# Kernel optimization log

Measured on AMD Instinct MI355X. Metric: run time of the kernel, lower is better.

Reference implementation:

```python
import jax, jax.numpy as jnp
import numpy as np

B, F, Q, CHUNK = 2, 8192, 4096, 512
NUM_VERTS = 6000


def _safe_div(n, d):
    return n / jnp.where(d == 0, 1.0, d)


def _bary(a, b, c, p):
    """Barycentric coords of the closest point on triangle (a,b,c) to p.
    All args broadcastable [..., 3]; returns [..., 3] (u, v, w) with
    closest = u*a + v*b + w*c. Ericson, Real-Time Collision Detection."""
    ab = b - a; ac = c - a; ap = p - a
    d1 = jnp.sum(ab * ap, -1); d2 = jnp.sum(ac * ap, -1)
    bp = p - b
    d3 = jnp.sum(ab * bp, -1); d4 = jnp.sum(ac * bp, -1)
    cp_ = p - c
    d5 = jnp.sum(ab * cp_, -1); d6 = jnp.sum(ac * cp_, -1)
    vc = d1 * d4 - d3 * d2
    vb = d5 * d2 - d1 * d6
    va = d3 * d6 - d5 * d4
    v_ab = _safe_div(d1, d1 - d3)
    w_ac = _safe_div(d2, d2 - d6)
    w_bc = _safe_div(d4 - d3, (d4 - d3) + (d5 - d6))
    inv = _safe_div(1.0, va + vb + vc)
    v_in = vb * inv; w_in = vc * inv
    zero = jnp.zeros_like(d1); one = jnp.ones_like(d1)
    conds = [(d1 <= 0) & (d2 <= 0),
             (d3 >= 0) & (d4 <= d3),
             (vc <= 0) & (d1 >= 0) & (d3 <= 0),
             (d6 >= 0) & (d5 <= d6),
             (vb <= 0) & (d2 >= 0) & (d6 <= 0),
             (va <= 0) & (d4 >= d3) & (d5 >= d6)]
    u = jnp.select(conds, [one, zero, 1 - v_ab, zero, 1 - w_ac, zero], 1 - v_in - w_in)
    v = jnp.select(conds, [zero, one, v_ab, zero, zero, 1 - w_bc], v_in)
    w = jnp.select(conds, [zero, zero, zero, one, w_ac, w_bc], w_in)
    return jnp.stack([u, v, w], -1)


def _closest_faces(triangles, points, chunk=CHUNK):
    """Exact closest-triangle index per query point (replaces BVH search).
    triangles [B,F,3,3], points [B,Q,3] -> int32 [B,Q]."""
    tri = jax.lax.stop_gradient(triangles)
    pts = jax.lax.stop_gradient(points)
    bsz, nq = pts.shape[0], pts.shape[1]
    a = tri[:, :, 0]; b = tri[:, :, 1]; c = tri[:, :, 2]  # [B,F,3]

    def one_chunk(p_chunk):  # [B,CH,3]
        pa = p_chunk[:, :, None, :]                       # [B,CH,1,3]
        bc = _bary(a[:, None], b[:, None], c[:, None], pa)  # [B,CH,F,3]
        cp = (bc[..., 0:1] * a[:, None] + bc[..., 1:2] * b[:, None]
              + bc[..., 2:3] * c[:, None])                # [B,CH,F,3]
        d2 = jnp.sum((cp - pa) ** 2, -1)                  # [B,CH,F]
        return jnp.argmin(d2, axis=-1)                    # [B,CH]

    chunks = jnp.moveaxis(pts.reshape(bsz, nq // chunk, chunk, 3), 1, 0)
    idx = jax.lax.map(one_chunk, chunks)                  # [NC,B,CH]
    return jnp.moveaxis(idx, 0, 1).reshape(bsz, nq)


def setup_inputs() -> dict:
    key = jax.random.key(0)
    k1, k2, k3, k4, k5 = jax.random.split(key, 5)
    return {
        'triangles': jax.random.normal(k1, (B, F, 3, 3), dtype=jnp.float32),
        'points': jax.random.normal(k2, (B, Q, 3), dtype=jnp.float32),
        'normals': jax.random.normal(k3, (B, F, 3, 3), dtype=jnp.float32),
        'cmaps': jax.random.normal(k4, (B, F, 3, 3), dtype=jnp.float32),
        'faces': jax.random.randint(k5, (B, F, 3), 0, NUM_VERTS, dtype=jnp.int32),
    }


def reference(triangles, points, normals, cmaps, faces):
    closest_faces = _closest_faces(triangles, points)     # [B,Q]
    idx = closest_faces[:, :, None, None]
    tri_g = jnp.take_along_axis(triangles, idx, axis=1)   # [B,Q,3,3]
    nrm_g = jnp.take_along_axis(normals, idx, axis=1)
    cmp_g = jnp.take_along_axis(cmaps, idx, axis=1)
    bcs = _bary(tri_g[:, :, 0], tri_g[:, :, 1], tri_g[:, :, 2], points)  # [B,Q,3]
    bcs = jnp.clip(bcs, 0.0, 1.0)
    closest_points = jnp.einsum('bqk,bqkd->bqd', bcs, tri_g)
    closest_normals = jnp.einsum('bqk,bqkd->bqd', bcs, nrm_g)
    closest_cmaps = jnp.einsum('bqk,bqkd->bqd', bcs, cmp_g)
    residual = closest_points - points
    closest_fids = jnp.take_along_axis(faces, closest_faces[:, :, None], axis=1)  # [B,Q,3]
    closest_idx = jnp.take_along_axis(
        closest_fids, jnp.argmax(bcs, -1)[:, :, None], axis=2)[..., 0]            # [B,Q]
    return residual, closest_normals, closest_cmaps, closest_idx
```

## Files before the change

### kernel.cpp

```cpp
#include <hip/hip_runtime.h>
#include <float.h>

#define B_   2
#define F_   8192
#define Q_   4096
#define NC   128
#define FC   (F_/NC)
#define PTS  128
#define PPT  4

typedef float f2 __attribute__((ext_vector_type(2)));
typedef float f4u __attribute__((ext_vector_type(4), aligned(4)));
typedef unsigned int uint;

__device__ __forceinline__ f2 clamp01(f2 x) {
    f2 z = {0.f, 0.f}, o = {1.f, 1.f};
    return __builtin_elementwise_min(__builtin_elementwise_max(x, z), o);
}

__device__ __forceinline__ void bary_uvw(
    float ax, float ay, float az,
    float bx, float by, float bz,
    float cx, float cy, float cz,
    float px, float py, float pz,
    float& u, float& v, float& w)
{
#pragma clang fp contract(off)
    float abx = bx - ax, aby = by - ay, abz = bz - az;
    float acx = cx - ax, acy = cy - ay, acz = cz - az;
    float apx = px - ax, apy = py - ay, apz = pz - az;
    float d1 = abx*apx + aby*apy + abz*apz;
    float d2 = acx*apx + acy*apy + acz*apz;
    float bpx = px - bx, bpy = py - by, bpz = pz - bz;
    float d3 = abx*bpx + aby*bpy + abz*bpz;
    float d4 = acx*bpx + acy*bpy + acz*bpz;
    float qx = px - cx, qy = py - cy, qz = pz - cz;
    float d5 = abx*qx + aby*qy + abz*qz;
    float d6 = acx*qx + acy*qy + acz*qz;
    float vc = d1*d4 - d3*d2;
    float vb = d5*d2 - d1*d6;
    float va = d3*d6 - d5*d4;

    bool c1 = (d1 <= 0.f) && (d2 <= 0.f);
    bool c2 = (d3 >= 0.f) && (d4 <= d3);
    bool c3 = (vc <= 0.f) && (d1 >= 0.f) && (d3 <= 0.f);
    bool c4 = (d6 >= 0.f) && (d5 <= d6);
    bool c5 = (vb <= 0.f) && (d2 >= 0.f) && (d6 <= 0.f);
    bool c6 = (va <= 0.f) && (d4 >= d3) && (d5 >= d6);

    bool e1 = c1;
    bool p1 = !c1;
    bool e2 = p1 && c2;
    bool p2 = p1 && !c2;
    bool e3 = p2 && c3;
    bool p3 = p2 && !c3;
    bool e4 = p3 && c4;
    bool p4 = p3 && !c4;
    bool e5 = p4 && c5;
    bool p5 = p4 && !c5;
    bool e6 = p5 && c6;

    float d43 = d4 - d3;
    float d56 = d5 - d6;
    float n  = e3 ? d1        : (e5 ? d2        : (e6 ? d43         : 1.f));
    float dd = e3 ? (d1 - d3) : (e5 ? (d2 - d6) : (e6 ? (d43 + d56) : (va + vb + vc)));
    dd = (dd == 0.f) ? 1.f : dd;
    float t = n / dd;

    float vi = vb * t;
    float wi = vc * t;
    u = e1 ? 1.f : (e2 ? 0.f : (e3 ? 1.f - t : (e4 ? 0.f : (e5 ? 1.f - t : (e6 ? 0.f     : 1.f - vi - wi)))));
    v = e1 ? 0.f : (e2 ? 1.f : (e3 ? t       : (e4 ? 0.f : (e5 ? 0.f     : (e6 ? 1.f - t : vi)))));
    w = e1 ? 0.f : (e2 ? 0.f : (e3 ? 0.f     : (e4 ? 1.f : (e5 ? t       : (e6 ? t       : wi)))));
}

__device__ __forceinline__ f2 pair_dist(
    f2 px, f2 py, f2 pz,
    float ax, float ay, float az,
    float abx, float aby, float abz,
    float acx, float acy, float acz,
    float daa, float dcc, float dac, float dbc, float kk,
    float rdaa, float rdcc, float rdbc, float rnn)
{
    f2 apx = px - ax, apy = py - ay, apz = pz - az;
    f2 d1  = abx*apx + aby*apy + abz*apz;
    f2 d2  = acx*apx + acy*apy + acz*apz;
    f2 app = apx*apx + apy*apy + apz*apz;

    f2 t1 = d1*dcc - d2*dac;
    f2 t2 = d2*daa - d1*dac;
    f2 t12n = 1.f - (t1 + t2)*rnn;
    f2 sgr  = (d1*t1 + d2*t2)*rnn;
    f2 ins  = __builtin_elementwise_min(__builtin_elementwise_min(t1, t2), t12n);

    f2 td1 = d1 + d1;
    f2 tab = clamp01(d1 * rdaa);
    f2 rab = tab*(td1 - tab*daa);
    f2 tac = clamp01(d2 * rdcc);
    f2 rac = tac*((d2 + d2) - tac*dcc);
    f2 d43 = (d2 - d1) + kk;
    f2 sbc = clamp01(d43 * rdbc);
    f2 rbc = (td1 - daa) + sbc*((d43 + d43) - sbc*dbc);
    f2 rmax = __builtin_elementwise_max(__builtin_elementwise_max(rab, rac), rbc);

    f2 red;
    red.x = (ins.x >= 0.f) ? sgr.x : rmax.x;
    red.y = (ins.y >= 0.f) ? sgr.y : rmax.y;
    f2 z = {0.f, 0.f};
    return __builtin_elementwise_max(app - red, z);
}

__global__ __launch_bounds__(PTS, 4) void scan_kernel(
    const float* __restrict__ tri, const float* __restrict__ pts,
    uint2* __restrict__ keys)
{
    __shared__ float4 S[FC * 4];
    const int tid = threadIdx.x;
    const int pb = blockIdx.x, cb = blockIdx.y, bb = blockIdx.z;

    {
        const int tr = tid & (FC - 1);
        const int hf = tid >> 6;
        const float* g = tri + ((size_t)bb * F_ + (size_t)cb * FC + tr) * 9;
        float ax = g[0], ay = g[1], az = g[2];
        float bx = g[3], by = g[4], bz = g[5];
        float cx = g[6], cy = g[7], cz = g[8];
        float abx = bx - ax, aby = by - ay, abz = bz - az;
        float acx = cx - ax, acy = cy - ay, acz = cz - az;
        float daa = abx*abx + aby*aby + abz*abz;
        float dcc = acx*acx + acy*acy + acz*acz;
        float dac = abx*acx + aby*acy + abz*acz;
        if (hf == 0) {
            S[tr*4 + 0] = make_float4(ax, ay, az, daa);
            S[tr*4 + 2] = make_float4(acx, acy, acz, dac);
        } else {
            float dbc = daa + dcc - 2.f*dac;
            float nn  = daa*dcc - dac*dac;
            S[tr*4 + 1] = make_float4(abx, aby, abz, dcc);
            S[tr*4 + 3] = make_float4(1.f/daa, 1.f/dcc, 1.f/dbc, 1.f/nn);
        }
    }
    __syncthreads();

    const int q0 = pb * (PTS * PPT) + tid * PPT;
    const float* p0 = pts + ((size_t)bb * Q_ + q0) * 3;
    f4u l0 = *(const f4u*)(p0);
    f4u l1 = *(const f4u*)(p0 + 4);
    f4u l2 = *(const f4u*)(p0 + 8);
    f2 pxA = {l0.x, l0.w}, pyA = {l0.y, l1.x}, pzA = {l0.z, l1.y};
    f2 pxB = {l1.z, l2.y}, pyB = {l1.w, l2.z}, pzB = {l2.x, l2.w};

    uint k00 = 0xFFFFFFFFu, k01 = 0xFFFFFFFFu;
    uint k10 = 0xFFFFFFFFu, k11 = 0xFFFFFFFFu;
    uint k20 = 0xFFFFFFFFu, k21 = 0xFFFFFFFFu;
    uint k30 = 0xFFFFFFFFu, k31 = 0xFFFFFFFFu;
    #pragma unroll 2
    for (int fl = 0; fl < FC; ++fl) {
        float4 c0 = S[fl*4 + 0];
        float4 c1 = S[fl*4 + 1];
        float4 c2 = S[fl*4 + 2];
        float4 c3 = S[fl*4 + 3];
        float daa = c0.w, dcc = c1.w, dac = c2.w;
        float dbc = daa + dcc - 2.f*dac;
        float kk  = daa - dac;

        f2 dA = pair_dist(pxA, pyA, pzA, c0.x, c0.y, c0.z,
                          c1.x, c1.y, c1.z, c2.x, c2.y, c2.z,
                          daa, dcc, dac, dbc, kk, c3.x, c3.y, c3.z, c3.w);
        f2 dB = pair_dist(pxB, pyB, pzB, c0.x, c0.y, c0.z,
                          c1.x, c1.y, c1.z, c2.x, c2.y, c2.z,
                          daa, dcc, dac, dbc, kk, c3.x, c3.y, c3.z, c3.w);

        uint kA0 = (__float_as_uint(dA.x) & 0xFFFFFFC0u) | (uint)fl;
        uint kA1 = (__float_as_uint(dA.y) & 0xFFFFFFC0u) | (uint)fl;
        uint kB0 = (__float_as_uint(dB.x) & 0xFFFFFFC0u) | (uint)fl;
        uint kB1 = (__float_as_uint(dB.y) & 0xFFFFFFC0u) | (uint)fl;
        uint lo, hi;
        lo = min(k00, kA0); hi = max(k00, kA0); k00 = lo; k01 = min(k01, hi);
        lo = min(k10, kA1); hi = max(k10, kA1); k10 = lo; k11 = min(k11, hi);
        lo = min(k20, kB0); hi = max(k20, kB0); k20 = lo; k21 = min(k21, hi);
        lo = min(k30, kB1); hi = max(k30, kB1); k30 = lo; k31 = min(k31, hi);
    }

    size_t idx = ((size_t)(bb * NC + cb) * Q_ + q0);
    uint4* k4 = (uint4*)&keys[idx];
    k4[0] = make_uint4(k00, k01, k10, k11);
    k4[1] = make_uint4(k20, k21, k30, k31);
}

__global__ __launch_bounds__(256) void finalize_kernel(
    const float* __restrict__ tri, const float* __restrict__ pts,
    const float* __restrict__ nrm, const float* __restrict__ cmp,
    const int* __restrict__ faces,
    const uint2* __restrict__ keys,
    float* __restrict__ out)
{
#pragma clang fp contract(off)
    const int lane = threadIdx.x & 63;
    const int t = blockIdx.x * 4 + (threadIdx.x >> 6);
    const int bb = t >> 12;
    const int q  = t & (Q_ - 1);

    const float* pp = pts + (size_t)t * 3;
    float px = pp[0], py = pp[1], pz = pp[2];

    uint2 kc0 = keys[((size_t)(bb * NC + 2*lane    ) * Q_ + q)];
    uint2 kc1 = keys[((size_t)(bb * NC + 2*lane + 1) * Q_ + q)];

    int face[4];
    face[0] = (2*lane    ) * FC + (int)(kc0.x & 63u);
    face[1] = (2*lane    ) * FC + (int)(kc0.y & 63u);
    face[2] = (2*lane + 1) * FC + (int)(kc1.x & 63u);
    face[3] = (2*lane + 1) * FC + (int)(kc1.y & 63u);

    f4u A[4], Bv[4]; float Cs[4];
    #pragma unroll
    for (int j = 0; j < 4; ++j) {
        const float* tg = tri + ((size_t)bb * F_ + face[j]) * 9;
        A[j]  = *(const f4u*)(tg);
        Bv[j] = *(const f4u*)(tg + 4);
        Cs[j] = tg[8];
    }

    float dbest = FLT_MAX; int fbest = 0x7FFFFFFF;
    #pragma unroll
    for (int j = 0; j < 4; ++j) {
        float ax = A[j].x, ay = A[j].y, az = A[j].z;
        float bx = A[j].w, by = Bv[j].x, bz = Bv[j].y;
        float cx = Bv[j].z, cy = Bv[j].w, cz = Cs[j];
        float u, v, w;
        bary_uvw(ax, ay, az, bx, by, bz, cx, cy, cz, px, py, pz, u, v, w);
        float cpx = u*ax + v*bx + w*cx;
        float cpy = u*ay + v*by + w*cy;
        float cpz = u*az + v*bz + w*cz;
        float dx = cpx - px, dy = cpy - py, dz = cpz - pz;
        float d2v = dx*dx + dy*dy + dz*dz;
        int fj = face[j];
        if (d2v < dbest || (d2v == dbest && fj < fbest)) { dbest = d2v; fbest = fj; }
    }
    for (int off = 32; off > 0; off >>= 1) {
        float od = __shfl_down(dbest, off);
        int   of = __shfl_down(fbest, off);
        if (od < dbest || (od == dbest && of < fbest)) { dbest = od; fbest = of; }
    }
    fbest = __shfl(fbest, 0);
    if (lane != 0) return;

    const int bestf = fbest;
    const float* tg = tri + ((size_t)bb * F_ + bestf) * 9;
    const float* ng = nrm + ((size_t)bb * F_ + bestf) * 9;
    const float* cg = cmp + ((size_t)bb * F_ + bestf) * 9;
    f4u TA = *(const f4u*)(tg), TB = *(const f4u*)(tg + 4);
    float TC = tg[8];
    f4u NA = *(const f4u*)(ng), NB = *(const f4u*)(ng + 4);
    float NCs = ng[8];
    f4u CA = *(const f4u*)(cg), CB = *(const f4u*)(cg + 4);
    float CC = cg[8];

    float u, v, w;
    bary_uvw(TA.x, TA.y, TA.z, TA.w, TB.x, TB.y, TB.z, TB.w, TC,
             px, py, pz, u, v, w);
    u = fminf(fmaxf(u, 0.f), 1.f);
    v = fminf(fmaxf(v, 0.f), 1.f);
    w = fminf(fmaxf(w, 0.f), 1.f);

    float cpx = u * TA.x + v * TA.w + w * TB.z;
    float cpy = u * TA.y + v * TB.x + w * TB.w;
    float cpz = u * TA.z + v * TB.y + w * TC;
    float nx  = u * NA.x + v * NA.w + w * NB.z;
    float ny  = u * NA.y + v * NB.x + w * NB.w;
    float nz  = u * NA.z + v * NB.y + w * NCs;
    float mx  = u * CA.x + v * CA.w + w * CB.z;
    float my  = u * CA.y + v * CB.x + w * CB.w;
    float mz  = u * CA.z + v * CB.y + w * CC;

    const size_t S3 = (size_t)B_ * Q_ * 3;
    out[(size_t)t * 3 + 0] = cpx - px;
    out[(size_t)t * 3 + 1] = cpy - py;
    out[(size_t)t * 3 + 2] = cpz - pz;
    out[S3 + (size_t)t * 3 + 0] = nx;
    out[S3 + (size_t)t * 3 + 1] = ny;
    out[S3 + (size_t)t * 3 + 2] = nz;
    out[2 * S3 + (size_t)t * 3 + 0] = mx;
    out[2 * S3 + (size_t)t * 3 + 1] = my;
    out[2 * S3 + (size_t)t * 3 + 2] = mz;

    int k = 0; float mm = u;
    if (v > mm) { mm = v; k = 1; }
    if (w > mm) { k = 2; }
    out[3 * S3 + t] = (float)faces[((size_t)bb * F_ + bestf) * 3 + k];
}

extern "C" void kernel_launch(void* const* d_in, const int* in_sizes, int n_in,
                              void* d_out, int out_size, void* d_ws, size_t ws_size,
                              hipStream_t stream) {
    const float* tri   = (const float*)d_in[0];
    const float* pts   = (const float*)d_in[1];
    const float* nrm   = (const float*)d_in[2];
    const float* cmp   = (const float*)d_in[3];
    const int*   faces = (const int*)d_in[4];
    float* out = (float*)d_out;

    uint2* keys = (uint2*)d_ws;

    dim3 g1(Q_ / (PTS * PPT), NC, B_);
    scan_kernel<<<g1, PTS, 0, stream>>>(tri, pts, keys);
    finalize_kernel<<<(B_ * Q_) / 4, 256, 0, stream>>>(
        tri, pts, nrm, cmp, faces, keys, out);
}
```

Baseline: 148.1 us.

## Move exact candidate refinement into scan kernel and transpose key layout

The scan kernel now refines its two approximate candidates per point with the exact barycentric distance, using triangle vertices cached in shared memory. It writes one (distance, face) pair per chunk in a point-major layout, so finalize does a single coalesced uint4 load per lane instead of gathering triangles from global memory and recomputing. The block size is doubled to 256 points, which halves the number of blocks and changes occupancy. The extra exact work in scan is small, but the per-point key writes are strided by NC and may coalesce poorly.

```diff
diff --git a/kernel.cpp b/kernel.cpp
--- a/kernel.cpp
+++ b/kernel.cpp
@@ -6,7 +6,7 @@
 #define Q_   4096
 #define NC   128
 #define FC   (F_/NC)
-#define PTS  128
+#define PTS  256
 #define PPT  4
 
 typedef float f2 __attribute__((ext_vector_type(2)));
@@ -114,14 +114,12 @@
     const float* __restrict__ tri, const float* __restrict__ pts,
     uint2* __restrict__ keys)
 {
-    __shared__ float4 S[FC * 4];
+    __shared__ float4 S[FC * 6];
     const int tid = threadIdx.x;
     const int pb = blockIdx.x, cb = blockIdx.y, bb = blockIdx.z;
 
-    {
-        const int tr = tid & (FC - 1);
-        const int hf = tid >> 6;
-        const float* g = tri + ((size_t)bb * F_ + (size_t)cb * FC + tr) * 9;
+    if (tid < FC) {
+        const float* g = tri + ((size_t)bb * F_ + (size_t)cb * FC + tid) * 9;
         float ax = g[0], ay = g[1], az = g[2];
         float bx = g[3], by = g[4], bz = g[5];
         float cx = g[6], cy = g[7], cz = g[8];
@@ -130,15 +128,14 @@
         float daa = abx*abx + aby*aby + abz*abz;
         float dcc = acx*acx + acy*acy + acz*acz;
         float dac = abx*acx + aby*acy + abz*acz;
-        if (hf == 0) {
-            S[tr*4 + 0] = make_float4(ax, ay, az, daa);
-            S[tr*4 + 2] = make_float4(acx, acy, acz, dac);
-        } else {
-            float dbc = daa + dcc - 2.f*dac;
-            float nn  = daa*dcc - dac*dac;
-            S[tr*4 + 1] = make_float4(abx, aby, abz, dcc);
-            S[tr*4 + 3] = make_float4(1.f/daa, 1.f/dcc, 1.f/dbc, 1.f/nn);
-        }
+        float dbc = daa + dcc - 2.f*dac;
+        float nn  = daa*dcc - dac*dac;
+        S[tid*6 + 0] = make_float4(ax, ay, az, daa);
+        S[tid*6 + 1] = make_float4(abx, aby, abz, dcc);
+        S[tid*6 + 2] = make_float4(acx, acy, acz, dac);
+        S[tid*6 + 3] = make_float4(1.f/daa, 1.f/dcc, 1.f/dbc, 1.f/nn);
+        S[tid*6 + 4] = make_float4(bx, by, bz, 0.f);
+        S[tid*6 + 5] = make_float4(cx, cy, cz, 0.f);
     }
     __syncthreads();
 
@@ -156,10 +153,10 @@
     uint k30 = 0xFFFFFFFFu, k31 = 0xFFFFFFFFu;
     #pragma unroll 2
     for (int fl = 0; fl < FC; ++fl) {
-        float4 c0 = S[fl*4 + 0];
-        float4 c1 = S[fl*4 + 1];
-        float4 c2 = S[fl*4 + 2];
-        float4 c3 = S[fl*4 + 3];
+        float4 c0 = S[fl*6 + 0];
+        float4 c1 = S[fl*6 + 1];
+        float4 c2 = S[fl*6 + 2];
+        float4 c3 = S[fl*6 + 3];
         float daa = c0.w, dcc = c1.w, dac = c2.w;
         float dbc = daa + dcc - 2.f*dac;
         float kk  = daa - dac;
@@ -182,10 +179,39 @@
         lo = min(k30, kB1); hi = max(k30, kB1); k30 = lo; k31 = min(k31, hi);
     }
 
-    size_t idx = ((size_t)(bb * NC + cb) * Q_ + q0);
-    uint4* k4 = (uint4*)&keys[idx];
-    k4[0] = make_uint4(k00, k01, k10, k11);
-    k4[1] = make_uint4(k20, k21, k30, k31);
+    float pxs[4] = {l0.x, l0.w, l1.z, l2.y};
+    float pys[4] = {l0.y, l1.x, l1.w, l2.z};
+    float pzs[4] = {l0.z, l1.y, l2.x, l2.w};
+    uint kk0[4] = {k00, k10, k20, k30};
+    uint kk1[4] = {k01, k11, k21, k31};
+
+    #pragma unroll
+    for (int p = 0; p < 4; ++p) {
+        float px = pxs[p], py = pys[p], pz = pzs[p];
+        float dbest = FLT_MAX; int fbest = 0x7FFFFFFF;
+        #pragma unroll
+        for (int j = 0; j < 2; ++j) {
+            int lf = (int)((j == 0 ? kk0[p] : kk1[p]) & 63u);
+            float4 ra = S[lf*6 + 0];
+            float4 rb = S[lf*6 + 4];
+            float4 rc = S[lf*6 + 5];
+            float u, v, w;
+            bary_uvw(ra.x, ra.y, ra.z, rb.x, rb.y, rb.z, rc.x, rc.y, rc.z,
+                     px, py, pz, u, v, w);
+            float d2v;
+            {
+#pragma clang fp contract(off)
+                float cpx = u*ra.x + v*rb.x + w*rc.x;
+                float cpy = u*ra.y + v*rb.y + w*rc.y;
+                float cpz = u*ra.z + v*rb.z + w*rc.z;
+                float dx = cpx - px, dy = cpy - py, dz = cpz - pz;
+                d2v = dx*dx + dy*dy + dz*dz;
+            }
+            int face = cb * FC + lf;
+            if (d2v < dbest || (d2v == dbest && face < fbest)) { dbest = d2v; fbest = face; }
+        }
+        keys[((size_t)bb * Q_ + q0 + p) * NC + cb] = make_uint2(__float_as_uint(dbest), (uint)fbest);
+    }
 }
 
 __global__ __launch_bounds__(256) void finalize_kernel(
@@ -199,52 +225,20 @@
     const int lane = threadIdx.x & 63;
     const int t = blockIdx.x * 4 + (threadIdx.x >> 6);
     const int bb = t >> 12;
-    const int q  = t & (Q_ - 1);
-
-    const float* pp = pts + (size_t)t * 3;
-    float px = pp[0], py = pp[1], pz = pp[2];
-
-    uint2 kc0 = keys[((size_t)(bb * NC + 2*lane    ) * Q_ + q)];
-    uint2 kc1 = keys[((size_t)(bb * NC + 2*lane + 1) * Q_ + q)];
-
-    int face[4];
-    face[0] = (2*lane    ) * FC + (int)(kc0.x & 63u);
-    face[1] = (2*lane    ) * FC + (int)(kc0.y & 63u);
-    face[2] = (2*lane + 1) * FC + (int)(kc1.x & 63u);
-    face[3] = (2*lane + 1) * FC + (int)(kc1.y & 63u);
-
-    f4u A[4], Bv[4]; float Cs[4];
-    #pragma unroll
-    for (int j = 0; j < 4; ++j) {
-        const float* tg = tri + ((size_t)bb * F_ + face[j]) * 9;
-        A[j]  = *(const f4u*)(tg);
-        Bv[j] = *(const f4u*)(tg + 4);
-        Cs[j] = tg[8];
-    }
-
-    float dbest = FLT_MAX; int fbest = 0x7FFFFFFF;
-    #pragma unroll
-    for (int j = 0; j < 4; ++j) {
-        float ax = A[j].x, ay = A[j].y, az = A[j].z;
-        float bx = A[j].w, by = Bv[j].x, bz = Bv[j].y;
-        float cx = Bv[j].z, cy = Bv[j].w, cz = Cs[j];
-        float u, v, w;
-        bary_uvw(ax, ay, az, bx, by, bz, cx, cy, cz, px, py, pz, u, v, w);
-        float cpx = u*ax + v*bx + w*cx;
-        float cpy = u*ay + v*by + w*cy;
-        float cpz = u*az + v*bz + w*cz;
-        float dx = cpx - px, dy = cpy - py, dz = cpz - pz;
-        float d2v = dx*dx + dy*dy + dz*dz;
-        int fj = face[j];
-        if (d2v < dbest || (d2v == dbest && fj < fbest)) { dbest = d2v; fbest = fj; }
-    }
+
+    uint4 K = ((const uint4*)keys)[(size_t)t * (NC/2) + lane];
+    float dbest = __uint_as_float(K.x); int fbest = (int)K.y;
+    float d1v   = __uint_as_float(K.z); int f1v   = (int)K.w;
+    if (d1v < dbest || (d1v == dbest && f1v < fbest)) { dbest = d1v; fbest = f1v; }
     for (int off = 32; off > 0; off >>= 1) {
         float od = __shfl_down(dbest, off);
         int   of = __shfl_down(fbest, off);
         if (od < dbest || (od == dbest && of < fbest)) { dbest = od; fbest = of; }
     }
-    fbest = __shfl(fbest, 0);
     if (lane != 0) return;
+
+    const float* pp = pts + (size_t)t * 3;
+    float px = pp[0], py = pp[1], pz = pp[2];
 
     const int bestf = fbest;
     const float* tg = tri + ((size_t)bb * F_ + bestf) * 9;
```

Measured after the change: 141.5 us, median of 2. -4.5%, faster.
